# Optimization experiments

Measured on AMD Instinct MI355X. Metric: run time of the kernel, lower is better.

Reference implementation:

```python
import jax, jax.numpy as jnp
import numpy as np

N = 100000      # nodes
E = 3200000     # edges (avg degree 32)
IN = 256        # in_channels
HID = 32        # hidden (hard-coded in module)
OUT = 40        # out_channels / classes
BN_EPS = 1e-5


def gcn_conv(x, W, b, src, dst, n):
    # PyG GCNConv: h = x @ W; add self-loops; symmetric norm D^-1/2 A D^-1/2; aggregate; + bias
    h = x @ W                                   # [n, d_out]
    loop = jnp.arange(n)
    s = jnp.concatenate([src, loop])            # [E+n]
    d = jnp.concatenate([dst, loop])
    deg = jax.ops.segment_sum(jnp.ones_like(d, dtype=h.dtype), d, num_segments=n)
    dinv = jnp.where(deg > 0, jax.lax.rsqrt(deg), 0.0)
    norm = dinv[s] * dinv[d]                    # [E+n]
    msg = h[s] * norm[:, None]                  # gather + scale
    return jax.ops.segment_sum(msg, d, num_segments=n) + b


def setup_inputs() -> dict:
    key = jax.random.key(0)
    k = jax.random.split(key, 4)
    x = jax.random.normal(k[0], (N, IN), dtype=jnp.float32)
    edge_index = jax.random.randint(k[1], (2, E), 0, N, dtype=jnp.int64)
    W1 = jax.random.normal(k[2], (IN, HID), dtype=jnp.float32) / np.float32(np.sqrt(IN))
    b1 = jnp.zeros((HID,), jnp.float32)
    W2 = jax.random.normal(k[3], (HID, OUT), dtype=jnp.float32) / np.float32(np.sqrt(HID))
    b2 = jnp.zeros((OUT,), jnp.float32)
    return {"x": x, "edge_index": edge_index, "W1": W1, "b1": b1, "W2": W2, "b2": b2}


def reference(x, edge_index, W1, b1, W2, b2):
    src, dst = edge_index[0], edge_index[1]
    h = jax.nn.elu(gcn_conv(x, W1, b1, src, dst, N))
    # BatchNorm1d created fresh each forward: batch stats, gamma=1, beta=0 (biased var)
    mean = jnp.mean(h, axis=0)
    var = jnp.mean((h - mean) ** 2, axis=0)
    h = (h - mean) * jax.lax.rsqrt(var + BN_EPS)
    h = jax.nn.relu(h)
    # Dropout(p=0.2): identity in eval / deterministic reference
    out = gcn_conv(h, W2, b2, src, dst, N)
    return jax.nn.log_softmax(out, axis=-1)
```

## Files before the change

kernel.cpp:

```cpp
#include <hip/hip_runtime.h>
#include <math.h>

typedef unsigned int uint;
typedef unsigned short ushort;
typedef float v2f __attribute__((ext_vector_type(2)));

__device__ __forceinline__ v2f fp8lo_to_f32(uint u) {
    return __builtin_amdgcn_cvt_pk_f32_fp8((int)u, false);
}
__device__ __forceinline__ v2f fp8hi_to_f32(uint u) {
    return __builtin_amdgcn_cvt_pk_f32_fp8((int)u, true);
}
__device__ __forceinline__ ushort f32x2_to_fp8(float a, float b) {
    return (ushort)(__builtin_amdgcn_cvt_pk_fp8_f32(a, b, 0, false) & 0xffff);
}

#define UNPACK8(r, f)                                                  \
    {                                                                  \
        v2f p0_ = fp8lo_to_f32((r).x), p1_ = fp8hi_to_f32((r).x);      \
        v2f p2_ = fp8lo_to_f32((r).y), p3_ = fp8hi_to_f32((r).y);      \
        f[0] += p0_.x; f[1] += p0_.y; f[2] += p1_.x; f[3] += p1_.y;    \
        f[4] += p2_.x; f[5] += p2_.y; f[6] += p3_.x; f[7] += p3_.y;    \
    }

#define NBU 49
#define CELL 9216
#define BUCK_CAP (8 * CELL)

__global__ __launch_bounds__(256) void k_bin(
    const int* __restrict__ src, const int* __restrict__ dst,
    int* __restrict__ cur, uint* __restrict__ ebuf, int E) {
    __shared__ int hist[NBU], base_[NBU], off[NBU];
    int tid = threadIdx.x;
    if (tid < NBU) { hist[tid] = 0; off[tid] = 0; }
    __syncthreads();
    int e0 = blockIdx.x * 4096 + tid;
    int s_[16], d_[16];
#pragma unroll
    for (int j = 0; j < 16; ++j) {
        int e = e0 + j * 256;
        if (e < E) {
            s_[j] = src[e]; d_[j] = dst[e];
            atomicAdd(&hist[d_[j] >> 11], 1);
        } else d_[j] = -1;
    }
    __syncthreads();
    int seg = blockIdx.x & 7;
    if (tid < NBU && hist[tid])
        base_[tid] = atomicAdd(&cur[tid * 8 + seg], hist[tid]);
    __syncthreads();
#pragma unroll
    for (int j = 0; j < 16; ++j) {
        if (d_[j] >= 0) {
            int b = d_[j] >> 11;
            int p = base_[b] + atomicAdd(&off[b], 1);
            if (p < CELL)
                ebuf[(size_t)(b * 8 + seg) * CELL + p] =
                    ((uint)(d_[j] & 2047) << 17) | (uint)s_[j];
        }
    }
}

__global__ __launch_bounds__(1024) void k_sort(
    const int* __restrict__ cur, const uint* __restrict__ ebuf,
    uint* __restrict__ csr, int* __restrict__ rowstart, int* __restrict__ deg,
    float* __restrict__ dinv, int n) {
    __shared__ int cnt[2048];
    __shared__ int part[1024];
    int tid = threadIdx.x, b = blockIdx.x;
    cnt[2 * tid] = 0; cnt[2 * tid + 1] = 0;
    __syncthreads();
    int lens[8];
    for (int s = 0; s < 8; ++s) {
        int len = cur[b * 8 + s]; if (len > CELL) len = CELL; lens[s] = len;
        const uint* ep = ebuf + (size_t)(b * 8 + s) * CELL;
        for (int i = tid; i < len; i += 1024)
            atomicAdd(&cnt[ep[i] >> 17], 1);
    }
    __syncthreads();
    int c0 = cnt[2 * tid], c1 = cnt[2 * tid + 1];
    part[tid] = c0 + c1;
    __syncthreads();
    for (int o = 1; o < 1024; o <<= 1) {
        int v = (tid >= o) ? part[tid - o] : 0;
        __syncthreads();
        part[tid] += v;
        __syncthreads();
    }
    int excl = (tid == 0) ? 0 : part[tid - 1];
    int bucketBase = b * BUCK_CAP;
    int node0 = b * 2048 + 2 * tid;
    if (node0 < n) {
        rowstart[node0] = bucketBase + excl;
        deg[node0] = c0;
        dinv[node0] = rsqrtf((float)c0 + 1.0f);
    }
    if (node0 + 1 < n) {
        rowstart[node0 + 1] = bucketBase + excl + c0;
        deg[node0 + 1] = c1;
        dinv[node0 + 1] = rsqrtf((float)c1 + 1.0f);
    }
    __syncthreads();
    cnt[2 * tid] = excl;
    cnt[2 * tid + 1] = excl + c0;
    __syncthreads();
    for (int s = 0; s < 8; ++s) {
        const uint* ep = ebuf + (size_t)(b * 8 + s) * CELL;
        int len = lens[s];
        for (int i = tid; i < len; i += 1024) {
            uint v = ep[i];
            int p = atomicAdd(&cnt[v >> 17], 1);
            csr[bucketBase + p] = v & 0x1FFFFu;
        }
    }
}


__global__ __launch_bounds__(256) void k_gemm1(
    const float* __restrict__ x, const float* __restrict__ W,
    const float* __restrict__ dinv, ushort* __restrict__ h8, int n) {
    __shared__ float part[4 * 32 * 64];
    int lane = threadIdx.x & 63;
    int wv = __builtin_amdgcn_readfirstlane(threadIdx.x >> 6);
    int node0 = blockIdx.x * 64;
    int node = node0 + lane;
    int koff = wv * 64;

    float acc[32];
#pragma unroll
    for (int c = 0; c < 32; ++c) acc[c] = 0.f;
    if (node < n) {
        const float4* xr = (const float4*)(x + (size_t)node * 256 + koff);
#pragma unroll 4
        for (int j4 = 0; j4 < 16; ++j4) {
            float4 xv = xr[j4];
            const float* w0 = W + (koff + j4 * 4) * 32;
#pragma unroll
            for (int c = 0; c < 32; ++c) acc[c] += xv.x * w0[c];
#pragma unroll
            for (int c = 0; c < 32; ++c) acc[c] += xv.y * w0[32 + c];
#pragma unroll
            for (int c = 0; c < 32; ++c) acc[c] += xv.z * w0[64 + c];
#pragma unroll
            for (int c = 0; c < 32; ++c) acc[c] += xv.w * w0[96 + c];
        }
    }
    float* pw = part + wv * 2048 + lane;
#pragma unroll
    for (int c = 0; c < 32; ++c) pw[c * 64] = acc[c];
    __syncthreads();

    int rn = threadIdx.x >> 2;
    int cq = threadIdx.x & 3;
    int dnode = node0 + rn;
    if (dnode < n) {
        float di = dinv[dnode];
        ushort us[4];
#pragma unroll
        for (int half = 0; half < 4; ++half) {
            float v0 = 0.f, v1 = 0.f;
#pragma unroll
            for (int w = 0; w < 4; ++w) {
                v0 += part[w * 2048 + (cq * 8 + half * 2 + 0) * 64 + rn];
                v1 += part[w * 2048 + (cq * 8 + half * 2 + 1) * 64 + rn];
            }
            us[half] = f32x2_to_fp8(v0 * di, v1 * di);
        }
        uint2 p;
        p.x = (uint)us[0] | ((uint)us[1] << 16);
        p.y = (uint)us[2] | ((uint)us[3] << 16);
        *(uint2*)(h8 + (size_t)dnode * 16 + cq * 4) = p;
    }
}

__global__ __launch_bounds__(256) void k_agg1(
    const ushort* __restrict__ hs, const int* __restrict__ deg,
    const int* __restrict__ rowstart, const uint* __restrict__ csr,
    const float* __restrict__ dinv, const float* __restrict__ b1,
    ushort* __restrict__ y, float* __restrict__ partials, int n) {
    int tid = threadIdx.x;
    int l4 = tid & 3;
    int g  = tid >> 2;
    int d  = blockIdx.x * 64 + g;
    float sa[8], qa[8];
#pragma unroll
    for (int j = 0; j < 8; ++j) { sa[j] = 0.f; qa[j] = 0.f; }
    if (d < n) {
        float a[8], c[8];
#pragma unroll
        for (int j = 0; j < 8; ++j) { a[j] = 0.f; c[j] = 0.f; }
        uint2 sr = *((const uint2*)(hs + (size_t)d * 16) + l4);
        UNPACK8(sr, a);
        const uint* row = csr + rowstart[d];
        int end = deg[d];
        int k = 0;
        for (; k + 4 <= end; k += 4) {
            uint s0 = row[k], s1 = row[k+1], s2 = row[k+2], s3 = row[k+3];
            uint2 r0 = *((const uint2*)(hs + (size_t)s0 * 16) + l4);
            uint2 r1 = *((const uint2*)(hs + (size_t)s1 * 16) + l4);
            uint2 r2 = *((const uint2*)(hs + (size_t)s2 * 16) + l4);
            uint2 r3 = *((const uint2*)(hs + (size_t)s3 * 16) + l4);
            UNPACK8(r0, a); UNPACK8(r1, c);
            UNPACK8(r2, a); UNPACK8(r3, c);
        }
        for (; k < end; ++k) {
            uint2 r = *((const uint2*)(hs + (size_t)row[k] * 16) + l4);
            UNPACK8(r, a);
        }
        float di = dinv[d];
        float4 bA = *(const float4*)(b1 + l4 * 8);
        float4 bB = *(const float4*)(b1 + l4 * 8 + 4);
        float bv[8] = {bA.x, bA.y, bA.z, bA.w, bB.x, bB.y, bB.z, bB.w};
        float vv[8];
#pragma unroll
        for (int j = 0; j < 8; ++j) {
            float v = di * (a[j] + c[j]) + bv[j];
            v = v > 0.f ? v : expm1f(v);
            vv[j] = v; sa[j] = v; qa[j] = v * v;
        }
        ushort u0 = f32x2_to_fp8(vv[0], vv[1]);
        ushort u1 = f32x2_to_fp8(vv[2], vv[3]);
        ushort u2 = f32x2_to_fp8(vv[4], vv[5]);
        ushort u3 = f32x2_to_fp8(vv[6], vv[7]);
        uint2 pw;
        pw.x = (uint)u0 | ((uint)u1 << 16);
        pw.y = (uint)u2 | ((uint)u3 << 16);
        *((uint2*)(y + (size_t)d * 16) + l4) = pw;
    }
#pragma unroll
    for (int m = 4; m <= 32; m <<= 1) {
#pragma unroll
        for (int j = 0; j < 8; ++j) {
            sa[j] += __shfl_xor(sa[j], m, 64);
            qa[j] += __shfl_xor(qa[j], m, 64);
        }
    }
    __shared__ float wred[4][4][16];
    int lane = tid & 63, wv = tid >> 6;
    if (lane < 4) {
#pragma unroll
        for (int j = 0; j < 8; ++j) {
            wred[wv][lane][j]     = sa[j];
            wred[wv][lane][8 + j] = qa[j];
        }
    }
    __syncthreads();
    if (tid < 64) {
        int l4g = tid >> 4, slot = tid & 15;
        partials[(size_t)blockIdx.x * 64 + tid] =
            wred[0][l4g][slot] + wred[1][l4g][slot] +
            wred[2][l4g][slot] + wred[3][l4g][slot];
    }
}

__global__ __launch_bounds__(1024) void k_red(
    const float* __restrict__ partials, float* __restrict__ stats, int nblk) {
    __shared__ float red[1024];
    int t = threadIdx.x;
    int j = t & 63, w = t >> 6;
    float a = 0.f;
    for (int i = w; i < nblk; i += 16) a += partials[(size_t)i * 64 + j];
    red[t] = a;
    __syncthreads();
    if (t < 64) {
        float v = 0.f;
#pragma unroll
        for (int kk = 0; kk < 16; ++kk) v += red[kk * 64 + t];
        int l4g = t >> 4, slot = t & 15, c = l4g * 8 + (slot & 7);
        stats[(slot < 8) ? c : (32 + c)] = v;
    }
}

__global__ void k_bn2(const ushort* __restrict__ y, const float* __restrict__ stats,
                      const float* __restrict__ dinv, ushort* __restrict__ h2s, int n) {
    int t = blockIdx.x * blockDim.x + threadIdx.x;
    if (t >= n * 16) return;
    int i = t >> 4, c2 = (t & 15) * 2;
    float invn = 1.0f / (float)n;
    float m0 = stats[c2] * invn,    m1 = stats[c2+1] * invn;
    float v0 = stats[32+c2] * invn - m0*m0;
    float v1 = stats[33+c2] * invn - m1*m1;
    float s0 = rsqrtf(v0 + 1e-5f), s1 = rsqrtf(v1 + 1e-5f);
    float di = dinv[i];
    v2f u = fp8lo_to_f32(y[t]);
    float a = (u.x - m0) * s0; a = a > 0.f ? a : 0.f; a *= di;
    float b = (u.y - m1) * s1; b = b > 0.f ? b : 0.f; b *= di;
    h2s[t] = f32x2_to_fp8(a, b);
}

__global__ __launch_bounds__(256) void k_agg2(
    const ushort* __restrict__ h2s, const int* __restrict__ deg,
    const int* __restrict__ rowstart, const uint* __restrict__ csr,
    const float* __restrict__ dinv, const float* __restrict__ W2,
    const float* __restrict__ b2, float* __restrict__ out, int n) {
    __shared__ float w2s[1280];
    __shared__ float b2s[40];
    __shared__ float tb[64][33];
    int tid = threadIdx.x;
    for (int t = tid; t < 1280; t += 256) w2s[t] = W2[t];
    if (tid < 40) b2s[tid] = b2[tid];
    int l4 = tid & 3, g = tid >> 2;
    int d = blockIdx.x * 64 + g;
    if (d < n) {
        float a[8], c[8];
#pragma unroll
        for (int j = 0; j < 8; ++j) { a[j] = 0.f; c[j] = 0.f; }
        uint2 sr = *((const uint2*)(h2s + (size_t)d * 16) + l4);
        UNPACK8(sr, a);
        const uint* row = csr + rowstart[d];
        int end = deg[d];
        int k = 0;
        for (; k + 4 <= end; k += 4) {
            uint s0 = row[k], s1 = row[k+1], s2 = row[k+2], s3 = row[k+3];
            uint2 r0 = *((const uint2*)(h2s + (size_t)s0 * 16) + l4);
            uint2 r1 = *((const uint2*)(h2s + (size_t)s1 * 16) + l4);
            uint2 r2 = *((const uint2*)(h2s + (size_t)s2 * 16) + l4);
            uint2 r3 = *((const uint2*)(h2s + (size_t)s3 * 16) + l4);
            UNPACK8(r0, a); UNPACK8(r1, c);
            UNPACK8(r2, a); UNPACK8(r3, c);
        }
        for (; k < end; ++k) {
            uint2 r = *((const uint2*)(h2s + (size_t)row[k] * 16) + l4);
            UNPACK8(r, a);
        }
        float di = dinv[d];
#pragma unroll
        for (int j = 0; j < 8; ++j) tb[g][l4 * 8 + j] = di * (a[j] + c[j]);
    }
    __syncthreads();
    float o[10];
    const float* bp = b2s + l4 * 10;
#pragma unroll
    for (int m = 0; m < 10; ++m) o[m] = bp[m];
#pragma unroll
    for (int cc = 0; cc < 32; ++cc) {
        float tc = tb[g][cc];
        const float* wr = w2s + cc * 40 + l4 * 10;
#pragma unroll
        for (int m = 0; m < 10; ++m) o[m] += tc * wr[m];
    }
    float mx = o[0];
#pragma unroll
    for (int m = 1; m < 10; ++m) mx = fmaxf(mx, o[m]);
    mx = fmaxf(mx, __shfl_xor(mx, 1, 64));
    mx = fmaxf(mx, __shfl_xor(mx, 2, 64));
    float s = 0.f;
#pragma unroll
    for (int m = 0; m < 10; ++m) s += __expf(o[m] - mx);
    s += __shfl_xor(s, 1, 64);
    s += __shfl_xor(s, 2, 64);
    float lse = mx + __logf(s);
    if (d < n) {
        float* r = out + (size_t)d * 40 + l4 * 10;
#pragma unroll
        for (int m = 0; m < 10; m += 2) {
            float2 wv;
            wv.x = o[m] - lse; wv.y = o[m+1] - lse;
            *(float2*)(r + m) = wv;
        }
    }
}


extern "C" void kernel_launch(void* const* d_in, const int* in_sizes, int n_in,
                              void* d_out, int out_size, void* d_ws, size_t ws_size,
                              hipStream_t stream) {
    const float* x  = (const float*)d_in[0];
    const int*   ei = (const int*)d_in[1];
    const float* W1 = (const float*)d_in[2];
    const float* b1 = (const float*)d_in[3];
    const float* W2 = (const float*)d_in[4];
    const float* b2 = (const float*)d_in[5];

    int n = in_sizes[0] / 256;
    int E = in_sizes[1] / 2;
    const int* src = ei;
    const int* dst = ei + E;

    char*   base    = (char*)d_ws;
    ushort* hs8     = (ushort*)base;
    ushort* y       = (ushort*)(base + (size_t)n * 32);
    ushort* h2s     = (ushort*)(base + (size_t)n * 64);
    float*  dinv    = (float*) (base + (size_t)n * 96);
    int*    deg     = (int*)   (base + (size_t)n * 100);
    int*    rowstart= (int*)   (base + (size_t)n * 104);
    float*  stats   = (float*) (base + (size_t)n * 108);
    int*    cur     = (int*)   (base + (size_t)n * 108 + 256);
    float*  partials= (float*) (base + (size_t)n * 108 + 2304);
    uint*   ebuf    = (uint*)  (base + (size_t)n * 108 + 2304 + 524288);
    size_t  ebufB   = (size_t)NBU * 8 * CELL * 4;
    uint*   csr     = (uint*)  ((char*)ebuf + ebufB);
    float*  out     = (float*)d_out;

    const int B = 256;
    int nb64 = (n + 63) / 64;

    hipMemsetAsync(cur, 0, NBU * 8 * sizeof(int), stream);

    k_bin <<<(E + 4095) / 4096, B, 0, stream>>>(src, dst, cur, ebuf, E);
    k_sort<<<NBU, 1024, 0, stream>>>(cur, ebuf, csr, rowstart, deg, dinv, n);

    k_gemm1<<<(n + 63) / 64, B, 0, stream>>>(x, W1, dinv, hs8, n);
    k_agg1 <<<nb64, B, 0, stream>>>(hs8, deg, rowstart, csr, dinv, b1, y,
                                    partials, n);
    k_red  <<<1, 1024, 0, stream>>>(partials, stats, nb64);

    k_bn2<<<(n * 16 + B - 1) / B, B, 0, stream>>>(y, stats, dinv, h2s, n);

    k_agg2<<<nb64, B, 0, stream>>>(h2s, deg, rowstart, csr, dinv, W2, b2, out, n);
}
```

Before: 407.3 us.

## Split per-bucket CSR sort into eight node-slice blocks for wider parallelism

The sort kernel previously ran one 1024-thread block per destination bucket, only 49 blocks in total. It now launches eight 256-thread blocks per bucket, each owning a 256-node slice with its own CSR capacity region. Each block rescans the whole bucket and keeps only the edges for its slice, using a wave-shuffle scan instead of a long shared-memory scan, with 4-way unrolled loads. This fills far more compute units at the cost of reading each bucket eight times, which should mostly hit cache. It also adds a per-slice capacity cap that could drop edges if a slice overflows.

```diff
diff --git a/kernel.cpp b/kernel.cpp
--- a/kernel.cpp
+++ b/kernel.cpp
@@ -25,7 +25,8 @@
 
 #define NBU 49
 #define CELL 9216
-#define BUCK_CAP (8 * CELL)
+#define SCAP2 9216
+#define BUCK_CAP (8 * SCAP2)
 
 __global__ __launch_bounds__(256) void k_bin(
     const int* __restrict__ src, const int* __restrict__ dst,
@@ -61,56 +62,88 @@
     }
 }
 
-__global__ __launch_bounds__(1024) void k_sort(
+__global__ __launch_bounds__(256) void k_sort2(
     const int* __restrict__ cur, const uint* __restrict__ ebuf,
     uint* __restrict__ csr, int* __restrict__ rowstart, int* __restrict__ deg,
     float* __restrict__ dinv, int n) {
-    __shared__ int cnt[2048];
-    __shared__ int part[1024];
-    int tid = threadIdx.x, b = blockIdx.x;
-    cnt[2 * tid] = 0; cnt[2 * tid + 1] = 0;
+    __shared__ int hist[256];
+    __shared__ int wsum[4];
+    int tid = threadIdx.x;
+    int b = blockIdx.x >> 3;
+    uint sl = blockIdx.x & 7;
+    hist[tid] = 0;
     __syncthreads();
     int lens[8];
     for (int s = 0; s < 8; ++s) {
         int len = cur[b * 8 + s]; if (len > CELL) len = CELL; lens[s] = len;
         const uint* ep = ebuf + (size_t)(b * 8 + s) * CELL;
-        for (int i = tid; i < len; i += 1024)
-            atomicAdd(&cnt[ep[i] >> 17], 1);
-    }
-    __syncthreads();
-    int c0 = cnt[2 * tid], c1 = cnt[2 * tid + 1];
-    part[tid] = c0 + c1;
-    __syncthreads();
-    for (int o = 1; o < 1024; o <<= 1) {
-        int v = (tid >= o) ? part[tid - o] : 0;
-        __syncthreads();
-        part[tid] += v;
-        __syncthreads();
-    }
-    int excl = (tid == 0) ? 0 : part[tid - 1];
-    int bucketBase = b * BUCK_CAP;
-    int node0 = b * 2048 + 2 * tid;
-    if (node0 < n) {
-        rowstart[node0] = bucketBase + excl;
-        deg[node0] = c0;
-        dinv[node0] = rsqrtf((float)c0 + 1.0f);
-    }
-    if (node0 + 1 < n) {
-        rowstart[node0 + 1] = bucketBase + excl + c0;
-        deg[node0 + 1] = c1;
-        dinv[node0 + 1] = rsqrtf((float)c1 + 1.0f);
-    }
-    __syncthreads();
-    cnt[2 * tid] = excl;
-    cnt[2 * tid + 1] = excl + c0;
+        int i = tid;
+        for (; i + 768 < len; i += 1024) {
+            uint v0 = ep[i], v1 = ep[i + 256], v2 = ep[i + 512], v3 = ep[i + 768];
+            if ((v0 >> 25) == sl) atomicAdd(&hist[(v0 >> 17) & 255], 1);
+            if ((v1 >> 25) == sl) atomicAdd(&hist[(v1 >> 17) & 255], 1);
+            if ((v2 >> 25) == sl) atomicAdd(&hist[(v2 >> 17) & 255], 1);
+            if ((v3 >> 25) == sl) atomicAdd(&hist[(v3 >> 17) & 255], 1);
+        }
+        for (; i < len; i += 256) {
+            uint v = ep[i];
+            if ((v >> 25) == sl) atomicAdd(&hist[(v >> 17) & 255], 1);
+        }
+    }
+    __syncthreads();
+    int c = hist[tid];
+    int lane = tid & 63, w = tid >> 6;
+    int incl = c;
+#pragma unroll
+    for (int o = 1; o < 64; o <<= 1) {
+        int t = __shfl_up(incl, o, 64);
+        if (lane >= o) incl += t;
+    }
+    if (lane == 63) wsum[w] = incl;
+    __syncthreads();
+    int add = 0;
+#pragma unroll
+    for (int k = 0; k < 4; ++k) if (k < w) add += wsum[k];
+    int excl = incl - c + add;
+    int sliceBase = (int)blockIdx.x * SCAP2;
+    int node = b * 2048 + (int)sl * 256 + tid;
+    if (node < n) {
+        deg[node] = c;
+        dinv[node] = rsqrtf((float)c + 1.0f);
+        rowstart[node] = sliceBase + excl;
+    }
+    __syncthreads();
+    hist[tid] = excl;
     __syncthreads();
     for (int s = 0; s < 8; ++s) {
         const uint* ep = ebuf + (size_t)(b * 8 + s) * CELL;
         int len = lens[s];
-        for (int i = tid; i < len; i += 1024) {
+        int i = tid;
+        for (; i + 768 < len; i += 1024) {
+            uint v0 = ep[i], v1 = ep[i + 256], v2 = ep[i + 512], v3 = ep[i + 768];
+            if ((v0 >> 25) == sl) {
+                int p = atomicAdd(&hist[(v0 >> 17) & 255], 1);
+                if (p < SCAP2) csr[sliceBase + p] = v0 & 0x1FFFFu;
+            }
+            if ((v1 >> 25) == sl) {
+                int p = atomicAdd(&hist[(v1 >> 17) & 255], 1);
+                if (p < SCAP2) csr[sliceBase + p] = v1 & 0x1FFFFu;
+            }
+            if ((v2 >> 25) == sl) {
+                int p = atomicAdd(&hist[(v2 >> 17) & 255], 1);
+                if (p < SCAP2) csr[sliceBase + p] = v2 & 0x1FFFFu;
+            }
+            if ((v3 >> 25) == sl) {
+                int p = atomicAdd(&hist[(v3 >> 17) & 255], 1);
+                if (p < SCAP2) csr[sliceBase + p] = v3 & 0x1FFFFu;
+            }
+        }
+        for (; i < len; i += 256) {
             uint v = ep[i];
-            int p = atomicAdd(&cnt[v >> 17], 1);
-            csr[bucketBase + p] = v & 0x1FFFFu;
+            if ((v >> 25) == sl) {
+                int p = atomicAdd(&hist[(v >> 17) & 255], 1);
+                if (p < SCAP2) csr[sliceBase + p] = v & 0x1FFFFu;
+            }
         }
     }
 }
@@ -397,8 +430,8 @@
 
     hipMemsetAsync(cur, 0, NBU * 8 * sizeof(int), stream);
 
-    k_bin <<<(E + 4095) / 4096, B, 0, stream>>>(src, dst, cur, ebuf, E);
-    k_sort<<<NBU, 1024, 0, stream>>>(cur, ebuf, csr, rowstart, deg, dinv, n);
+    k_bin  <<<(E + 4095) / 4096, B, 0, stream>>>(src, dst, cur, ebuf, E);
+    k_sort2<<<NBU * 8, B, 0, stream>>>(cur, ebuf, csr, rowstart, deg, dinv, n);
 
     k_gemm1<<<(n + 63) / 64, B, 0, stream>>>(x, W1, dinv, hs8, n);
     k_agg1 <<<nb64, B, 0, stream>>>(hs8, deg, rowstart, csr, dinv, b1, y,
```

New measurement: 427.7 us. +5.0%, slower.
